# Performance work log

Measured on AMD Instinct MI355X. Metric: run time of the kernel, lower is better.

Reference implementation:

```python
import jax, jax.numpy as jnp
import numpy as np

B = 65536
SIZES = (1024, 512, 768)
OUT = 512
RANK = 10


def setup_inputs() -> dict:
    key = jax.random.key(0)
    ks = jax.random.split(key, 7)
    x1 = jax.random.normal(ks[0], (B, SIZES[0]), dtype=jnp.float32)
    x2 = jax.random.normal(ks[1], (B, SIZES[1]), dtype=jnp.float32)
    x3 = jax.random.normal(ks[2], (B, SIZES[2]), dtype=jnp.float32)
    # factor init ~ nn-style scaling so the Hadamard product doesn't blow up
    f1 = jax.random.normal(ks[3], (SIZES[0], RANK), dtype=jnp.float32) / np.sqrt(SIZES[0])
    f2 = jax.random.normal(ks[4], (SIZES[1], RANK), dtype=jnp.float32) / np.sqrt(SIZES[1])
    f3 = jax.random.normal(ks[5], (SIZES[2], RANK), dtype=jnp.float32) / np.sqrt(SIZES[2])
    f_out = jax.random.normal(ks[6], (OUT, RANK), dtype=jnp.float32) / np.sqrt(RANK)
    return {"x1": x1, "x2": x2, "x3": x3, "f1": f1, "f2": f2, "f3": f3, "f_out": f_out}


def reference(x1, x2, x3, f1, f2, f3, f_out):
    # y = (x1 @ f1) * (x2 @ f2) * (x3 @ f3) @ f_out.T   -- CP low-rank fusion
    y = (x1 @ f1) * (x2 @ f2) * (x3 @ f3)        # [B, RANK]
    return y @ f_out.T                            # [B, OUT]
```

## Files before the change

### kernel.cpp

```cpp
#include <hip/hip_runtime.h>
#include <cstdint>
#include <cstddef>

#define RANK 10

typedef float f2_t __attribute__((ext_vector_type(2)));
typedef float f4_t __attribute__((ext_vector_type(4)));

__global__ __launch_bounds__(256, 4)
void cp_fusion_kernel(const float* __restrict__ x1, const float* __restrict__ x2,
                      const float* __restrict__ x3, const float* __restrict__ f1,
                      const float* __restrict__ f2, const float* __restrict__ f3,
                      const float* __restrict__ fo, float* __restrict__ out)
{
    __shared__ float lds[8320];
    const int tid  = threadIdx.x;
    const int lane = tid & 63;
    const int wid  = __builtin_amdgcn_readfirstlane(tid >> 6);
    const int row_base = blockIdx.x << 6;

    const float* xs[3] = {x1, x2, x3};
    const float* fs[3] = {f1, f2, f3};
    const int    S [3] = {1024, 512, 768};
    const int    NC[3] = {8, 4, 6};

    float res[3][RANK];

    #pragma unroll
    for (int a = 0; a < 3; ++a) {
        const float* __restrict__ xa = xs[a];
        const float* __restrict__ fa = fs[a];
        const int stride = S[a];
        const int nc = NC[a];

        float acc[RANK];
        #pragma unroll
        for (int r = 0; r < RANK; ++r) acc[r] = 0.f;

        f2_t xpre[16];
        #pragma unroll
        for (int i = 0; i < 16; ++i) {
            const int e   = tid + (i << 8);
            const int row = e >> 6;
            const int col = (e & 63) << 1;
            xpre[i] = *(const f2_t*)&xa[(size_t)(row_base + row) * stride + col];
        }

        #pragma unroll 1
        for (int c = 0; c < nc; ++c) {
            __syncthreads();
            #pragma unroll
            for (int i = 0; i < 16; ++i) {
                const int e   = tid + (i << 8);
                const int row = e >> 6;
                const int col = (e & 63) << 1;
                *(f2_t*)&lds[row * 130 + col] = xpre[i];
            }
            if (c + 1 < nc) {
                const int jb = (c + 1) << 7;
                #pragma unroll
                for (int i = 0; i < 16; ++i) {
                    const int e   = tid + (i << 8);
                    const int row = e >> 6;
                    const int col = (e & 63) << 1;
                    xpre[i] = *(const f2_t*)&xa[(size_t)(row_base + row) * stride + jb + col];
                }
            }
            __syncthreads();

            const float* __restrict__ fptr = fa + (size_t)((c << 7) + wid * 32) * RANK;
            const float* __restrict__ xrow = &lds[lane * 130 + wid * 32];

            f4_t fb[2][5];
            #pragma unroll
            for (int p = 0; p < 5; ++p) fb[0][p] = *(const f4_t*)&fptr[p * 4];

            #pragma unroll
            for (int kp = 0; kp < 16; ++kp) {
                const int cur = kp & 1;
                if (kp < 15) {
                    const float* __restrict__ fnx = fptr + (kp + 1) * 20;
                    #pragma unroll
                    for (int p = 0; p < 5; ++p) fb[cur ^ 1][p] = *(const f4_t*)&fnx[p * 4];
                }
                const f2_t xv = *(const f2_t*)&xrow[kp << 1];
                const f4_t b0 = fb[cur][0], b1 = fb[cur][1], b2 = fb[cur][2],
                           b3 = fb[cur][3], b4 = fb[cur][4];
                acc[0] = fmaf(xv.x, b0.x, acc[0]);
                acc[1] = fmaf(xv.x, b0.y, acc[1]);
                acc[2] = fmaf(xv.x, b0.z, acc[2]);
                acc[3] = fmaf(xv.x, b0.w, acc[3]);
                acc[4] = fmaf(xv.x, b1.x, acc[4]);
                acc[5] = fmaf(xv.x, b1.y, acc[5]);
                acc[6] = fmaf(xv.x, b1.z, acc[6]);
                acc[7] = fmaf(xv.x, b1.w, acc[7]);
                acc[8] = fmaf(xv.x, b2.x, acc[8]);
                acc[9] = fmaf(xv.x, b2.y, acc[9]);
                acc[0] = fmaf(xv.y, b2.z, acc[0]);
                acc[1] = fmaf(xv.y, b2.w, acc[1]);
                acc[2] = fmaf(xv.y, b3.x, acc[2]);
                acc[3] = fmaf(xv.y, b3.y, acc[3]);
                acc[4] = fmaf(xv.y, b3.z, acc[4]);
                acc[5] = fmaf(xv.y, b3.w, acc[5]);
                acc[6] = fmaf(xv.y, b4.x, acc[6]);
                acc[7] = fmaf(xv.y, b4.y, acc[7]);
                acc[8] = fmaf(xv.y, b4.z, acc[8]);
                acc[9] = fmaf(xv.y, b4.w, acc[9]);
            }
        }
        #pragma unroll
        for (int r = 0; r < RANK; ++r) res[a][r] = acc[r];
    }

    __syncthreads();
    {
        const int pb = wid * 1920 + lane * 30;
        #pragma unroll
        for (int r = 0; r < RANK; ++r) {
            lds[pb + r]      = res[0][r];
            lds[pb + 10 + r] = res[1][r];
            lds[pb + 20 + r] = res[2][r];
        }
    }
    __syncthreads();
    if (tid < 64) {
        #pragma unroll
        for (int r = 0; r < RANK; ++r) {
            float va = 0.f, vb = 0.f, vc = 0.f;
            #pragma unroll
            for (int w = 0; w < 4; ++w) {
                const int pb = w * 1920 + tid * 30;
                va += lds[pb + r];
                vb += lds[pb + 10 + r];
                vc += lds[pb + 20 + r];
            }
            lds[7680 + tid * RANK + r] = va * vb * vc;
        }
    }
    __syncthreads();

    const int o0 = (tid & 127) << 2;
    const f4_t* __restrict__ fo4 = (const f4_t*)(fo + (size_t)o0 * RANK);
    f4_t fof[10];
    #pragma unroll
    for (int p = 0; p < 10; ++p) fof[p] = fo4[p];

    const float* y = lds + 7680;
    const int half = tid >> 7;
    #pragma unroll 2
    for (int i = 0; i < 32; ++i) {
        const int row = (i << 1) + half;
        float yv[RANK];
        #pragma unroll
        for (int r = 0; r < RANK; ++r) yv[r] = y[row * RANK + r];
        float4 o; o.x = 0.f; o.y = 0.f; o.z = 0.f; o.w = 0.f;
        #pragma unroll
        for (int d = 0; d < 4; ++d) {
            float s = 0.f;
            #pragma unroll
            for (int r = 0; r < RANK; ++r) {
                const int q = d * RANK + r;
                s = fmaf(yv[r], fof[q >> 2][q & 3], s);
            }
            if (d == 0) o.x = s; else if (d == 1) o.y = s;
            else if (d == 2) o.z = s; else o.w = s;
        }
        *(float4*)&out[(size_t)(row_base + row) * 512 + o0] = o;
    }
}

extern "C" void kernel_launch(void* const* d_in, const int* in_sizes, int n_in,
                              void* d_out, int out_size, void* d_ws, size_t ws_size,
                              hipStream_t stream) {
    const float* x1 = (const float*)d_in[0];
    const float* x2 = (const float*)d_in[1];
    const float* x3 = (const float*)d_in[2];
    const float* f1 = (const float*)d_in[3];
    const float* f2 = (const float*)d_in[4];
    const float* f3 = (const float*)d_in[5];
    const float* fo = (const float*)d_in[6];
    float* out = (float*)d_out;
    (void)in_sizes; (void)n_in; (void)out_size; (void)d_ws; (void)ws_size;

    dim3 grid(1024), block(256);
    hipLaunchKernelGGL(cp_fusion_kernel, grid, block, 0, stream,
                       x1, x2, x3, f1, f2, f3, fo, out);
}
```

Baseline: 632.1 us.

## Halve rows per block, prefetch next input across stages, reduce per stage

Each block now handles 32 rows instead of 64, with twice as many blocks, a smaller LDS footprint and launch bounds raised to 8 blocks per CU to increase occupancy. Each wave splits its K slice across two half-waves and combines them with a shuffle. The next input matrix is prefetched while the last chunk of the current one is processed, and the per-stage reduction now happens after each input instead of once at the end. Outputs use nontemporal stores. The trade-offs are more block-level syncs, dropped double-buffering of the factor loads, and reloading factor matrices from cache in twice as many blocks.

```diff
diff --git a/kernel.cpp b/kernel.cpp
--- a/kernel.cpp
+++ b/kernel.cpp
@@ -7,24 +7,36 @@
 typedef float f2_t __attribute__((ext_vector_type(2)));
 typedef float f4_t __attribute__((ext_vector_type(4)));
 
-__global__ __launch_bounds__(256, 4)
+__global__ __launch_bounds__(256, 8)
 void cp_fusion_kernel(const float* __restrict__ x1, const float* __restrict__ x2,
                       const float* __restrict__ x3, const float* __restrict__ f1,
                       const float* __restrict__ f2, const float* __restrict__ f3,
                       const float* __restrict__ fo, float* __restrict__ out)
 {
-    __shared__ float lds[8320];
+    __shared__ float lds[5120];
     const int tid  = threadIdx.x;
     const int lane = tid & 63;
     const int wid  = __builtin_amdgcn_readfirstlane(tid >> 6);
-    const int row_base = blockIdx.x << 6;
+    const int row_base = blockIdx.x << 5;
 
     const float* xs[3] = {x1, x2, x3};
     const float* fs[3] = {f1, f2, f3};
     const int    S [3] = {1024, 512, 768};
     const int    NC[3] = {8, 4, 6};
 
-    float res[3][RANK];
+    const int rrow = lane & 31;
+    const int cb   = wid * 32 + ((lane >> 5) << 4);
+
+    f4_t fof[10];
+
+    f2_t xpre[8];
+    #pragma unroll
+    for (int i = 0; i < 8; ++i) {
+        const int e   = tid + (i << 8);
+        const int row = e >> 6;
+        const int col = (e & 63) << 1;
+        xpre[i] = *(const f2_t*)&x1[(size_t)(row_base + row) * 1024 + col];
+    }
 
     #pragma unroll
     for (int a = 0; a < 3; ++a) {
@@ -37,20 +49,11 @@
         #pragma unroll
         for (int r = 0; r < RANK; ++r) acc[r] = 0.f;
 
-        f2_t xpre[16];
-        #pragma unroll
-        for (int i = 0; i < 16; ++i) {
-            const int e   = tid + (i << 8);
-            const int row = e >> 6;
-            const int col = (e & 63) << 1;
-            xpre[i] = *(const f2_t*)&xa[(size_t)(row_base + row) * stride + col];
-        }
-
         #pragma unroll 1
         for (int c = 0; c < nc; ++c) {
             __syncthreads();
             #pragma unroll
-            for (int i = 0; i < 16; ++i) {
+            for (int i = 0; i < 8; ++i) {
                 const int e   = tid + (i << 8);
                 const int row = e >> 6;
                 const int col = (e & 63) << 1;
@@ -59,33 +62,35 @@
             if (c + 1 < nc) {
                 const int jb = (c + 1) << 7;
                 #pragma unroll
-                for (int i = 0; i < 16; ++i) {
+                for (int i = 0; i < 8; ++i) {
                     const int e   = tid + (i << 8);
                     const int row = e >> 6;
                     const int col = (e & 63) << 1;
                     xpre[i] = *(const f2_t*)&xa[(size_t)(row_base + row) * stride + jb + col];
                 }
+            } else if (a < 2) {
+                const float* __restrict__ xn = xs[a + 1];
+                const int ns = S[a + 1];
+                #pragma unroll
+                for (int i = 0; i < 8; ++i) {
+                    const int e   = tid + (i << 8);
+                    const int row = e >> 6;
+                    const int col = (e & 63) << 1;
+                    xpre[i] = *(const f2_t*)&xn[(size_t)(row_base + row) * ns + col];
+                }
             }
             __syncthreads();
 
-            const float* __restrict__ fptr = fa + (size_t)((c << 7) + wid * 32) * RANK;
-            const float* __restrict__ xrow = &lds[lane * 130 + wid * 32];
-
-            f4_t fb[2][5];
+            const float* __restrict__ fptr = fa + (size_t)((c << 7) + cb) * RANK;
+            const float* __restrict__ xrow = &lds[rrow * 130 + cb];
             #pragma unroll
-            for (int p = 0; p < 5; ++p) fb[0][p] = *(const f4_t*)&fptr[p * 4];
-
-            #pragma unroll
-            for (int kp = 0; kp < 16; ++kp) {
-                const int cur = kp & 1;
-                if (kp < 15) {
-                    const float* __restrict__ fnx = fptr + (kp + 1) * 20;
-                    #pragma unroll
-                    for (int p = 0; p < 5; ++p) fb[cur ^ 1][p] = *(const f4_t*)&fnx[p * 4];
-                }
+            for (int kp = 0; kp < 8; ++kp) {
+                const f4_t b0 = *(const f4_t*)&fptr[kp * 20 +  0];
+                const f4_t b1 = *(const f4_t*)&fptr[kp * 20 +  4];
+                const f4_t b2 = *(const f4_t*)&fptr[kp * 20 +  8];
+                const f4_t b3 = *(const f4_t*)&fptr[kp * 20 + 12];
+                const f4_t b4 = *(const f4_t*)&fptr[kp * 20 + 16];
                 const f2_t xv = *(const f2_t*)&xrow[kp << 1];
-                const f4_t b0 = fb[cur][0], b1 = fb[cur][1], b2 = fb[cur][2],
-                           b3 = fb[cur][3], b4 = fb[cur][4];
                 acc[0] = fmaf(xv.x, b0.x, acc[0]);
                 acc[1] = fmaf(xv.x, b0.y, acc[1]);
                 acc[2] = fmaf(xv.x, b0.z, acc[2]);
@@ -108,52 +113,52 @@
                 acc[9] = fmaf(xv.y, b4.w, acc[9]);
             }
         }
+
         #pragma unroll
-        for (int r = 0; r < RANK; ++r) res[a][r] = acc[r];
+        for (int r = 0; r < RANK; ++r)
+            acc[r] += __shfl_xor(acc[r], 32);
+
+        if (a == 2) {
+            const int o0 = (tid & 127) << 2;
+            const f4_t* __restrict__ fo4 = (const f4_t*)(fo + (size_t)o0 * RANK);
+            #pragma unroll
+            for (int p = 0; p < 10; ++p) fof[p] = fo4[p];
+        }
+
+        __syncthreads();
+        if (lane < 32) {
+            #pragma unroll
+            for (int r = 0; r < RANK; ++r)
+                lds[wid * 320 + rrow * 10 + r] = acc[r];
+        }
+        __syncthreads();
+        if (tid < 32) {
+            #pragma unroll
+            for (int r = 0; r < RANK; ++r) {
+                const float s = lds[        tid * 10 + r] + lds[320 + tid * 10 + r]
+                              + lds[640 +  tid * 10 + r] + lds[960 + tid * 10 + r];
+                if (a == 0)      lds[4160 + tid * 10 + r] = s;
+                else if (a == 1) lds[4480 + tid * 10 + r] = s;
+                else {
+                    const float y0 = lds[4160 + tid * 10 + r];
+                    const float y1 = lds[4480 + tid * 10 + r];
+                    lds[4800 + tid * 10 + r] = y0 * y1 * s;
+                }
+            }
+        }
+        __syncthreads();
     }
 
-    __syncthreads();
-    {
-        const int pb = wid * 1920 + lane * 30;
-        #pragma unroll
-        for (int r = 0; r < RANK; ++r) {
-            lds[pb + r]      = res[0][r];
-            lds[pb + 10 + r] = res[1][r];
-            lds[pb + 20 + r] = res[2][r];
-        }
-    }
-    __syncthreads();
-    if (tid < 64) {
-        #pragma unroll
-        for (int r = 0; r < RANK; ++r) {
-            float va = 0.f, vb = 0.f, vc = 0.f;
-            #pragma unroll
-            for (int w = 0; w < 4; ++w) {
-                const int pb = w * 1920 + tid * 30;
-                va += lds[pb + r];
-                vb += lds[pb + 10 + r];
-                vc += lds[pb + 20 + r];
-            }
-            lds[7680 + tid * RANK + r] = va * vb * vc;
-        }
-    }
-    __syncthreads();
-
     const int o0 = (tid & 127) << 2;
-    const f4_t* __restrict__ fo4 = (const f4_t*)(fo + (size_t)o0 * RANK);
-    f4_t fof[10];
-    #pragma unroll
-    for (int p = 0; p < 10; ++p) fof[p] = fo4[p];
-
-    const float* y = lds + 7680;
+    const float* yb = lds + 4800;
     const int half = tid >> 7;
     #pragma unroll 2
-    for (int i = 0; i < 32; ++i) {
+    for (int i = 0; i < 16; ++i) {
         const int row = (i << 1) + half;
         float yv[RANK];
         #pragma unroll
-        for (int r = 0; r < RANK; ++r) yv[r] = y[row * RANK + r];
-        float4 o; o.x = 0.f; o.y = 0.f; o.z = 0.f; o.w = 0.f;
+        for (int r = 0; r < RANK; ++r) yv[r] = yb[row * RANK + r];
+        f4_t o = {0.f, 0.f, 0.f, 0.f};
         #pragma unroll
         for (int d = 0; d < 4; ++d) {
             float s = 0.f;
@@ -162,10 +167,9 @@
                 const int q = d * RANK + r;
                 s = fmaf(yv[r], fof[q >> 2][q & 3], s);
             }
-            if (d == 0) o.x = s; else if (d == 1) o.y = s;
-            else if (d == 2) o.z = s; else o.w = s;
+            o[d] = s;
         }
-        *(float4*)&out[(size_t)(row_base + row) * 512 + o0] = o;
+        __builtin_nontemporal_store(o, (f4_t*)&out[(size_t)(row_base + row) * 512 + o0]);
     }
 }
 
@@ -182,7 +186,7 @@
     float* out = (float*)d_out;
     (void)in_sizes; (void)n_in; (void)out_size; (void)d_ws; (void)ws_size;
 
-    dim3 grid(1024), block(256);
+    dim3 grid(2048), block(256);
     hipLaunchKernelGGL(cp_fusion_kernel, grid, block, 0, stream,
                        x1, x2, x3, f1, f2, f3, fo, out);
 }
```

Measured after the change: 1.064 ms. 1.68x slower.
